# Kernel optimization log

Measured on AMD Instinct MI355X. Metric: run time of the kernel, lower is better.

Reference implementation:

```python
import jax, jax.numpy as jnp
import numpy as np

EPS = 1e-6
NEG_SLOPE = 0.2

B, C_IN, N, K = 4, 64, 40960, 16
C_OUT = 64


def setup_inputs() -> dict:
    key = jax.random.key(0)
    k1, k2, k3 = jax.random.split(key, 3)
    feature = jax.random.normal(k1, (B, C_IN, N, 1), dtype=jnp.float32)
    neigh_idx = jax.random.randint(k2, (B, N, K), 0, N, dtype=jnp.int64)
    # 1x1 conv kernel [C_out, C_in] (kaiming-like scale), no bias since bn=True
    W = jax.random.normal(k3, (C_OUT, C_IN), dtype=jnp.float32) * np.float32(np.sqrt(2.0 / C_IN))
    gamma = jnp.ones((C_OUT,), dtype=jnp.float32)
    beta = jnp.zeros((C_OUT,), dtype=jnp.float32)
    return {"feature": feature, "W": W, "gamma": gamma, "beta": beta, "neigh_idx": neigh_idx}


def _gather_neighbour(pc, neigh_idx):
    # pc: [B, C, N]; neigh_idx: [B, N, K] -> [B, C, N, K]
    return jax.vmap(lambda p, idx: p[:, idx])(pc, neigh_idx)


def reference(feature, W, gamma, beta, neigh_idx):
    pc = feature[..., 0]                       # [B, C, N]
    f_neigh = _gather_neighbour(pc, neigh_idx) # [B, C, N, K]
    x = jnp.concatenate([feature, f_neigh], axis=-1)  # [B, C, N, K+1]
    # 1x1 conv (no bias)
    y = jnp.einsum('oc,bcnk->bonk', W, x)      # [B, C_out, N, K+1]
    # BatchNorm2d (training mode: batch stats over B,N,K+1), eps=1e-6
    mean = jnp.mean(y, axis=(0, 2, 3), keepdims=True)
    var = jnp.mean(jnp.square(y - mean), axis=(0, 2, 3), keepdims=True)
    yn = (y - mean) * jax.lax.rsqrt(var + EPS)
    yn = yn * gamma[None, :, None, None] + beta[None, :, None, None]
    # LeakyReLU(0.2)
    act = jnp.where(yn >= 0, yn, NEG_SLOPE * yn)
    # sum over neighbor axis, keepdim
    return jnp.sum(act, axis=-1, keepdims=True)  # [B, C_out, N, 1]
```

## Files before the change

### kernel.cpp

```cpp
#include <hip/hip_runtime.h>
#include <hip/hip_fp16.h>

typedef _Float16 h2 __attribute__((ext_vector_type(2)));

#define BB 4
#define CIN 64
#define COUT 64
#define NN 40960
#define KK 16
#define GBLK (BB * NN / 256)
#define FPAD 264
#define WPAD 68
#define HP 32
#define HR 2
#define HBINS (NN / HR)
#define HWORDS (HBINS / 4)

__global__ __launch_bounds__(256) void k_hist(const int* __restrict__ idx,
                                              unsigned int* __restrict__ hist,
                                              float* __restrict__ sums) {
    __shared__ unsigned int bins[HWORDS];
    const int tid = threadIdx.x;
    const int p = blockIdx.x >> 3;
    const int b = (blockIdx.x & 7) >> 1;
    const int r = blockIdx.x & 1;
    const int lo = r * HBINS;

    if (blockIdx.x == 0 && tid < 128) sums[tid] = 0.f;

#pragma unroll
    for (int i = 0; i < HWORDS / 256; ++i) bins[i * 256 + tid] = 0u;
    __syncthreads();

    const int SHARE = NN * KK / HP;
    const int4* src = (const int4*)(idx + (size_t)b * NN * KK + (size_t)p * SHARE);
#pragma unroll 4
    for (int i = 0; i < SHARE / 4 / 256; ++i) {
        int4 v = src[i * 256 + tid];
        unsigned a0 = (unsigned)(v.x - lo), a1 = (unsigned)(v.y - lo);
        unsigned a2 = (unsigned)(v.z - lo), a3 = (unsigned)(v.w - lo);
        if (a0 < HBINS) atomicAdd(&bins[a0 >> 2], 1u << ((a0 & 3) * 8));
        if (a1 < HBINS) atomicAdd(&bins[a1 >> 2], 1u << ((a1 & 3) * 8));
        if (a2 < HBINS) atomicAdd(&bins[a2 >> 2], 1u << ((a2 & 3) * 8));
        if (a3 < HBINS) atomicAdd(&bins[a3 >> 2], 1u << ((a3 & 3) * 8));
    }
    __syncthreads();
    unsigned int* dst = hist + (size_t)((b * HP + p) * HR + r) * HWORDS;
#pragma unroll
    for (int i = 0; i < HWORDS / 256; ++i) dst[i * 256 + tid] = bins[i * 256 + tid];
}

__global__ __launch_bounds__(256) void k_gemm(const float* __restrict__ feat,
                                              const float* __restrict__ W,
                                              const unsigned int* __restrict__ hist,
                                              __half* __restrict__ g,
                                              float* __restrict__ sums) {
    __shared__ float Wt_s[64 * WPAD];
    __shared__ float feat_s[16 * FPAD];
    __shared__ float w_s[256];

    const int tid   = threadIdx.x;
    const int b     = (blockIdx.x & 7) >> 1;
    const int chunk = (blockIdx.x & 1) * 80 + (blockIdx.x >> 3);
    const int n0    = chunk * 256;

    {
        const int n  = n0 + tid;
        const int r  = n / HBINS;
        const int ml = n - r * HBINS;
        const int w  = ml >> 2;
        const int sh = (ml & 3) * 8;
        unsigned s = 1u;
#pragma unroll
        for (int p = 0; p < HP; ++p)
            s += (hist[(size_t)((b * HP + p) * HR + r) * HWORDS + w] >> sh) & 0xffu;
        w_s[tid] = (float)s;
    }

#pragma unroll
    for (int it = 0; it < 16; ++it) {
        int c = tid & 63;
        int o = it * 4 + (tid >> 6);
        Wt_s[c * WPAD + o] = W[o * 64 + c];
    }

    const int to = tid & 7;
    const int tn = tid >> 3;

    float acc[8][8];
#pragma unroll
    for (int i = 0; i < 8; ++i)
#pragma unroll
        for (int j = 0; j < 8; ++j) acc[i][j] = 0.f;

    const float* fb = feat + (size_t)b * CIN * NN + n0;

    for (int cc0 = 0; cc0 < 64; cc0 += 16) {
        __syncthreads();
        {
            int row = tid >> 4;
            int col = (tid & 15) * 4;
            const float* src = fb + (size_t)(cc0 + row) * NN + col;
#pragma unroll
            for (int q = 0; q < 4; ++q) {
                float4 v = *(const float4*)(src + q * 64);
                *(float4*)&feat_s[row * FPAD + col + q * 64] = v;
            }
        }
        __syncthreads();

#pragma unroll
        for (int cc = 0; cc < 16; ++cc) {
            int c = cc0 + cc;
            float4 w0 = *(const float4*)&Wt_s[c * WPAD + to * 8];
            float4 w1 = *(const float4*)&Wt_s[c * WPAD + to * 8 + 4];
            float4 f0 = *(const float4*)&feat_s[cc * FPAD + tn * 8];
            float4 f1 = *(const float4*)&feat_s[cc * FPAD + tn * 8 + 4];
            float wv[8] = {w0.x, w0.y, w0.z, w0.w, w1.x, w1.y, w1.z, w1.w};
            float fv[8] = {f0.x, f0.y, f0.z, f0.w, f1.x, f1.y, f1.z, f1.w};
#pragma unroll
            for (int i = 0; i < 8; ++i)
#pragma unroll
                for (int j = 0; j < 8; ++j)
                    acc[i][j] = fmaf(wv[i], fv[j], acc[i][j]);
        }
    }

    __half* gb = g + ((size_t)b * NN + n0) * 64;
#pragma unroll
    for (int j = 0; j < 8; ++j) {
        int n = tn * 8 + j;
        union { uint4 u; h2 h[4]; } P;
#pragma unroll
        for (int h = 0; h < 4; ++h) {
            h2 t;
            t.x = (_Float16)acc[2 * h][j];
            t.y = (_Float16)acc[2 * h + 1][j];
            P.h[h] = t;
        }
        *(uint4*)&gb[(size_t)n * 64 + to * 8] = P.u;
    }

    float wgt[8];
#pragma unroll
    for (int j = 0; j < 8; ++j) wgt[j] = w_s[tn * 8 + j];
    float s1[8], s2[8];
#pragma unroll
    for (int i = 0; i < 8; ++i) { s1[i] = 0.f; s2[i] = 0.f; }
#pragma unroll
    for (int j = 0; j < 8; ++j)
#pragma unroll
        for (int i = 0; i < 8; ++i) {
            float wv = wgt[j] * acc[i][j];
            s1[i] += wv;
            s2[i] += wv * acc[i][j];
        }

    __syncthreads();
    float* red = feat_s;
#pragma unroll
    for (int i = 0; i < 8; ++i) {
        int o = to * 8 + i;
        red[o * 33 + tn]        = s1[i];
        red[2112 + o * 33 + tn] = s2[i];
    }
    __syncthreads();
    if (tid < 128) {
        int arr = tid >> 6, o = tid & 63;
        const float* base = red + arr * 2112 + o * 33;
        float s = 0.f;
#pragma unroll
        for (int t = 0; t < 32; ++t) s += base[t];
        atomicAdd(&sums[arr * 64 + o], s);
    }
}

__global__ __launch_bounds__(256) void k_final(const __half* __restrict__ g,
                                               const int* __restrict__ idx,
                                               const float* __restrict__ sums,
                                               const float* __restrict__ gamma,
                                               const float* __restrict__ beta,
                                               float* __restrict__ out) {
    const int tid  = threadIdx.x;
    const int lane = tid & 63;
    const int wave = tid >> 6;
    const int b     = (blockIdx.x & 7) >> 1;
    const int chunk = ((blockIdx.x >> 3) << 1) | (blockIdx.x & 1);
    const int n0    = chunk * 64;

    __shared__ int   idx_s[64 * 17];
    __shared__ float tile[64 * 65];
    __shared__ float prm[128];

    {
        const int4* src = (const int4*)(idx + ((size_t)b * NN + n0) * KK);
        int4 v = src[tid];
        int row = tid >> 2, col = (tid & 3) * 4;
        idx_s[row * 17 + col + 0] = v.x;
        idx_s[row * 17 + col + 1] = v.y;
        idx_s[row * 17 + col + 2] = v.z;
        idx_s[row * 17 + col + 3] = v.w;
    }

    if (tid < 64) {
        const double TOT = (double)BB * NN * (KK + 1);
        double mean = (double)sums[tid] / TOT;
        double var  = (double)sums[64 + tid] / TOT - mean * mean;
        double inv  = 1.0 / sqrt(var + 1e-6);
        float scale = (float)inv * gamma[tid];
        float shift = beta[tid] - (float)mean * scale;
        prm[tid]      = scale;
        prm[64 + tid] = shift;
    }
    __syncthreads();

    const int r  = lane >> 3;
    const int q8 = (lane & 7) * 8;
    h2 sc2[4], sh2[4];
#pragma unroll
    for (int h = 0; h < 4; ++h) {
        h2 a, s;
        a.x = (_Float16)prm[q8 + 2 * h];      a.y = (_Float16)prm[q8 + 2 * h + 1];
        s.x = (_Float16)prm[64 + q8 + 2 * h]; s.y = (_Float16)prm[64 + q8 + 2 * h + 1];
        sc2[h] = a; sh2[h] = s;
    }

    const __half* gb = g + (size_t)b * NN * 64;

#pragma unroll
    for (int rr = 0; rr < 2; ++rr) {
        const int nl = wave * 16 + rr * 8 + r;
        h2 acc[4];
#pragma unroll
        for (int h = 0; h < 4; ++h) acc[h] = (h2)(_Float16)0;

#pragma unroll
        for (int k = -1; k < KK; ++k) {
            int m = (k < 0) ? (n0 + nl) : idx_s[nl * 17 + k];
            union { uint4 u; h2 h[4]; } U;
            U.u = *(const uint4*)(gb + (size_t)m * 64 + q8);
#pragma unroll
            for (int h = 0; h < 4; ++h) {
                h2 t = U.h[h] * sc2[h] + sh2[h];
                acc[h] += __builtin_elementwise_max(t, t * (_Float16)0.2f);
            }
        }
        float* tr = &tile[nl * 65 + q8];
#pragma unroll
        for (int h = 0; h < 4; ++h) {
            tr[2 * h]     = (float)acc[h].x;
            tr[2 * h + 1] = (float)acc[h].y;
        }
    }
    __syncthreads();
    const int j   = tid & 63;
    const int sub = tid >> 6;
#pragma unroll
    for (int ob = 0; ob < 16; ++ob) {
        int o = ob * 4 + sub;
        out[(size_t)(b * 64 + o) * NN + n0 + j] = tile[j * 65 + o];
    }
}

extern "C" void kernel_launch(void* const* d_in, const int* in_sizes, int n_in,
                              void* d_out, int out_size, void* d_ws, size_t ws_size,
                              hipStream_t stream) {
    const float* feat  = (const float*)d_in[0];
    const float* W     = (const float*)d_in[1];
    const float* gamma = (const float*)d_in[2];
    const float* beta  = (const float*)d_in[3];
    const int*   idx   = (const int*)d_in[4];
    float* out = (float*)d_out;

    char* ws = (char*)d_ws;
    __half* g = (__half*)ws;
    size_t off = (size_t)BB * NN * 64 * sizeof(__half);
    unsigned int* hist = (unsigned int*)(ws + off);
    off += (size_t)BB * HP * HR * HWORDS * sizeof(unsigned int);
    float* sums = (float*)(ws + off);

    k_hist<<<BB * HP * HR, 256, 0, stream>>>(idx, hist, sums);
    k_gemm<<<GBLK, 256, 0, stream>>>(feat, W, hist, g, sums);
    k_final<<<(BB * NN) / 64, 256, 0, stream>>>(g, idx, sums, gamma, beta, out);
}
```

Before: 155.3 us.

## Split neighbour gathers into two index-range passes and use nontemporal idx/out access

The final kernel now gathers neighbour rows in two passes, each touching only neighbours whose index falls in one half of the point range. This is meant to shrink the live working set of the fp16 feature table so it stays resident in cache. Index loads and output stores become nontemporal so they do not evict the gathered table. The cost is a branch per neighbour, accumulators held for both rows at once, and divergent lanes inside each pass.

After: 186.3 us. 1.2x slower.

```diff
diff --git a/kernel.cpp b/kernel.cpp
--- a/kernel.cpp
+++ b/kernel.cpp
@@ -2,6 +2,7 @@
 #include <hip/hip_fp16.h>
 
 typedef _Float16 h2 __attribute__((ext_vector_type(2)));
+typedef unsigned int u32x4 __attribute__((ext_vector_type(4)));
 
 #define BB 4
 #define CIN 64
@@ -193,13 +194,13 @@
     __shared__ float prm[128];
 
     {
-        const int4* src = (const int4*)(idx + ((size_t)b * NN + n0) * KK);
-        int4 v = src[tid];
+        const u32x4* src = (const u32x4*)(idx + ((size_t)b * NN + n0) * KK);
+        u32x4 v = __builtin_nontemporal_load(src + tid);
         int row = tid >> 2, col = (tid & 3) * 4;
-        idx_s[row * 17 + col + 0] = v.x;
-        idx_s[row * 17 + col + 1] = v.y;
-        idx_s[row * 17 + col + 2] = v.z;
-        idx_s[row * 17 + col + 3] = v.w;
+        idx_s[row * 17 + col + 0] = (int)v.x;
+        idx_s[row * 17 + col + 1] = (int)v.y;
+        idx_s[row * 17 + col + 2] = (int)v.z;
+        idx_s[row * 17 + col + 3] = (int)v.w;
     }
 
     if (tid < 64) {
@@ -227,29 +228,43 @@
 
     const __half* gb = g + (size_t)b * NN * 64;
 
+    h2 acc[2][4];
+#pragma unroll
+    for (int rr = 0; rr < 2; ++rr)
+#pragma unroll
+        for (int h = 0; h < 4; ++h) acc[rr][h] = (h2)(_Float16)0;
+
+#pragma unroll
+    for (int pass = 0; pass < 2; ++pass) {
+        const int mlo = pass * (NN / 2);
+#pragma unroll
+        for (int rr = 0; rr < 2; ++rr) {
+            const int nl = wave * 16 + rr * 8 + r;
+#pragma unroll
+            for (int k = -1; k < KK; ++k) {
+                int m = (k < 0) ? (n0 + nl) : idx_s[nl * 17 + k];
+                if ((unsigned)(m - mlo) < (unsigned)(NN / 2)) {
+                    union { uint4 u; h2 h[4]; } U;
+                    U.u = *(const uint4*)(gb + (size_t)m * 64 + q8);
+#pragma unroll
+                    for (int h = 0; h < 4; ++h) {
+                        h2 t = U.h[h] * sc2[h] + sh2[h];
+                        acc[rr][h] += __builtin_elementwise_max(t, t * (_Float16)0.2f);
+                    }
+                }
+            }
+        }
+        __builtin_amdgcn_sched_barrier(0);
+    }
+
 #pragma unroll
     for (int rr = 0; rr < 2; ++rr) {
         const int nl = wave * 16 + rr * 8 + r;
-        h2 acc[4];
-#pragma unroll
-        for (int h = 0; h < 4; ++h) acc[h] = (h2)(_Float16)0;
-
-#pragma unroll
-        for (int k = -1; k < KK; ++k) {
-            int m = (k < 0) ? (n0 + nl) : idx_s[nl * 17 + k];
-            union { uint4 u; h2 h[4]; } U;
-            U.u = *(const uint4*)(gb + (size_t)m * 64 + q8);
-#pragma unroll
-            for (int h = 0; h < 4; ++h) {
-                h2 t = U.h[h] * sc2[h] + sh2[h];
-                acc[h] += __builtin_elementwise_max(t, t * (_Float16)0.2f);
-            }
-        }
         float* tr = &tile[nl * 65 + q8];
 #pragma unroll
         for (int h = 0; h < 4; ++h) {
-            tr[2 * h]     = (float)acc[h].x;
-            tr[2 * h + 1] = (float)acc[h].y;
+            tr[2 * h]     = (float)acc[rr][h].x;
+            tr[2 * h + 1] = (float)acc[rr][h].y;
         }
     }
     __syncthreads();
@@ -258,7 +273,8 @@
 #pragma unroll
     for (int ob = 0; ob < 16; ++ob) {
         int o = ob * 4 + sub;
-        out[(size_t)(b * 64 + o) * NN + n0 + j] = tile[j * 65 + o];
+        __builtin_nontemporal_store(tile[j * 65 + o],
+                                    &out[(size_t)(b * 64 + o) * NN + n0 + j]);
     }
 }
 
```

## Use fp16 MFMA for pointwise conv GEMM and add nontemporal idx/out accesses

Applied to the files above, without the earlier changes.

Replaces the fp32 register-tiled FMA GEMM in k_gemm with fp16 MFMA 16x16x32 instructions. W is loaded directly into fragments, and feature values are converted to half straight from global memory without an LDS staging loop. Results go through a padded LDS tile so the g stores stay coalesced, and the BN-stat reduction is reworked to match the MFMA output layout. k_final also switches the neighbour-index loads and output stores to nontemporal hints. Rounding the inputs and weights to fp16 before the matmul lowers precision of y and the batch statistics, and the feature loads become strided scalar reads.

Measured after the change: 158.4 us. 1.02x slower.

```diff
diff --git a/kernel.cpp b/kernel.cpp
--- a/kernel.cpp
+++ b/kernel.cpp
@@ -2,6 +2,9 @@
 #include <hip/hip_fp16.h>
 
 typedef _Float16 h2 __attribute__((ext_vector_type(2)));
+typedef _Float16 f16x8 __attribute__((ext_vector_type(8)));
+typedef float f32x4 __attribute__((ext_vector_type(4)));
+typedef unsigned int u32x4 __attribute__((ext_vector_type(4)));
 
 #define BB 4
 #define CIN 64
@@ -9,12 +12,11 @@
 #define NN 40960
 #define KK 16
 #define GBLK (BB * NN / 256)
-#define FPAD 264
-#define WPAD 68
 #define HP 32
 #define HR 2
 #define HBINS (NN / HR)
 #define HWORDS (HBINS / 4)
+#define GTP 72
 
 __global__ __launch_bounds__(256) void k_hist(const int* __restrict__ idx,
                                               unsigned int* __restrict__ hist,
@@ -55,9 +57,9 @@
                                               const unsigned int* __restrict__ hist,
                                               __half* __restrict__ g,
                                               float* __restrict__ sums) {
-    __shared__ float Wt_s[64 * WPAD];
-    __shared__ float feat_s[16 * FPAD];
-    __shared__ float w_s[256];
+    __shared__ __half gt[4][64][GTP];
+    __shared__ float  red[2][64][17];
+    __shared__ float  w_s[256];
 
     const int tid   = threadIdx.x;
     const int b     = (blockIdx.x & 7) >> 1;
@@ -77,101 +79,102 @@
         w_s[tid] = (float)s;
     }
 
-#pragma unroll
-    for (int it = 0; it < 16; ++it) {
-        int c = tid & 63;
-        int o = it * 4 + (tid >> 6);
-        Wt_s[c * WPAD + o] = W[o * 64 + c];
-    }
-
-    const int to = tid & 7;
-    const int tn = tid >> 3;
-
-    float acc[8][8];
-#pragma unroll
-    for (int i = 0; i < 8; ++i)
-#pragma unroll
-        for (int j = 0; j < 8; ++j) acc[i][j] = 0.f;
-
-    const float* fb = feat + (size_t)b * CIN * NN + n0;
-
-    for (int cc0 = 0; cc0 < 64; cc0 += 16) {
-        __syncthreads();
-        {
-            int row = tid >> 4;
-            int col = (tid & 15) * 4;
-            const float* src = fb + (size_t)(cc0 + row) * NN + col;
-#pragma unroll
-            for (int q = 0; q < 4; ++q) {
-                float4 v = *(const float4*)(src + q * 64);
-                *(float4*)&feat_s[row * FPAD + col + q * 64] = v;
+    const int wv = tid >> 6;
+    const int l  = tid & 63;
+    const int lr = l & 15;
+    const int lg = l >> 4;
+
+    f16x8 bf[2][4];
+#pragma unroll
+    for (int ot = 0; ot < 4; ++ot)
+#pragma unroll
+        for (int kc = 0; kc < 2; ++kc) {
+            const float* wp = W + (size_t)(ot * 16 + lr) * 64 + kc * 32 + lg * 8;
+            float4 w0 = *(const float4*)(wp);
+            float4 w1 = *(const float4*)(wp + 4);
+            f16x8 t;
+            t[0] = (_Float16)w0.x; t[1] = (_Float16)w0.y;
+            t[2] = (_Float16)w0.z; t[3] = (_Float16)w0.w;
+            t[4] = (_Float16)w1.x; t[5] = (_Float16)w1.y;
+            t[6] = (_Float16)w1.z; t[7] = (_Float16)w1.w;
+            bf[kc][ot] = t;
+        }
+
+    f32x4 acc[4][4];
+#pragma unroll
+    for (int i = 0; i < 4; ++i)
+#pragma unroll
+        for (int j = 0; j < 4; ++j) acc[i][j] = (f32x4)0.f;
+
+    const float* fb = feat + (size_t)b * CIN * NN;
+    const int nbase = n0 + wv * 64;
+
+#pragma unroll
+    for (int nt = 0; nt < 4; ++nt) {
+        const int n = nbase + nt * 16 + lr;
+#pragma unroll
+        for (int kc = 0; kc < 2; ++kc) {
+            const float* ap = fb + (size_t)(kc * 32 + lg * 8) * NN + n;
+            f16x8 a;
+#pragma unroll
+            for (int j = 0; j < 8; ++j) a[j] = (_Float16)ap[(size_t)j * NN];
+#pragma unroll
+            for (int ot = 0; ot < 4; ++ot)
+                acc[nt][ot] = __builtin_amdgcn_mfma_f32_16x16x32_f16(
+                    a, bf[kc][ot], acc[nt][ot], 0, 0, 0);
+        }
+    }
+
+    float wr[4][4];
+#pragma unroll
+    for (int nt = 0; nt < 4; ++nt)
+#pragma unroll
+        for (int r = 0; r < 4; ++r)
+            wr[nt][r] = w_s[wv * 64 + nt * 16 + lg * 4 + r];
+
+    float s1[4] = {0.f, 0.f, 0.f, 0.f}, s2[4] = {0.f, 0.f, 0.f, 0.f};
+#pragma unroll
+    for (int nt = 0; nt < 4; ++nt)
+#pragma unroll
+        for (int ot = 0; ot < 4; ++ot)
+#pragma unroll
+            for (int r = 0; r < 4; ++r) {
+                float y = acc[nt][ot][r];
+                float t = wr[nt][r] * y;
+                s1[ot] += t;
+                s2[ot] += t * y;
             }
-        }
-        __syncthreads();
-
-#pragma unroll
-        for (int cc = 0; cc < 16; ++cc) {
-            int c = cc0 + cc;
-            float4 w0 = *(const float4*)&Wt_s[c * WPAD + to * 8];
-            float4 w1 = *(const float4*)&Wt_s[c * WPAD + to * 8 + 4];
-            float4 f0 = *(const float4*)&feat_s[cc * FPAD + tn * 8];
-            float4 f1 = *(const float4*)&feat_s[cc * FPAD + tn * 8 + 4];
-            float wv[8] = {w0.x, w0.y, w0.z, w0.w, w1.x, w1.y, w1.z, w1.w};
-            float fv[8] = {f0.x, f0.y, f0.z, f0.w, f1.x, f1.y, f1.z, f1.w};
-#pragma unroll
-            for (int i = 0; i < 8; ++i)
-#pragma unroll
-                for (int j = 0; j < 8; ++j)
-                    acc[i][j] = fmaf(wv[i], fv[j], acc[i][j]);
-        }
-    }
+
+#pragma unroll
+    for (int nt = 0; nt < 4; ++nt)
+#pragma unroll
+        for (int ot = 0; ot < 4; ++ot)
+#pragma unroll
+            for (int r = 0; r < 4; ++r)
+                gt[wv][nt * 16 + lg * 4 + r][ot * 16 + lr] = (__half)acc[nt][ot][r];
+
+#pragma unroll
+    for (int ot = 0; ot < 4; ++ot) {
+        red[0][ot * 16 + lr][wv * 4 + lg] = s1[ot];
+        red[1][ot * 16 + lr][wv * 4 + lg] = s2[ot];
+    }
+    __syncthreads();
 
     __half* gb = g + ((size_t)b * NN + n0) * 64;
 #pragma unroll
-    for (int j = 0; j < 8; ++j) {
-        int n = tn * 8 + j;
-        union { uint4 u; h2 h[4]; } P;
-#pragma unroll
-        for (int h = 0; h < 4; ++h) {
-            h2 t;
-            t.x = (_Float16)acc[2 * h][j];
-            t.y = (_Float16)acc[2 * h + 1][j];
-            P.h[h] = t;
-        }
-        *(uint4*)&gb[(size_t)n * 64 + to * 8] = P.u;
-    }
-
-    float wgt[8];
-#pragma unroll
-    for (int j = 0; j < 8; ++j) wgt[j] = w_s[tn * 8 + j];
-    float s1[8], s2[8];
-#pragma unroll
-    for (int i = 0; i < 8; ++i) { s1[i] = 0.f; s2[i] = 0.f; }
-#pragma unroll
-    for (int j = 0; j < 8; ++j)
-#pragma unroll
-        for (int i = 0; i < 8; ++i) {
-            float wv = wgt[j] * acc[i][j];
-            s1[i] += wv;
-            s2[i] += wv * acc[i][j];
-        }
-
-    __syncthreads();
-    float* red = feat_s;
-#pragma unroll
     for (int i = 0; i < 8; ++i) {
-        int o = to * 8 + i;
-        red[o * 33 + tn]        = s1[i];
-        red[2112 + o * 33 + tn] = s2[i];
-    }
-    __syncthreads();
+        int nl = i * 32 + (tid >> 3);
+        int o8 = (tid & 7) * 8;
+        uint4 v = *(const uint4*)&gt[nl >> 6][nl & 63][o8];
+        *(uint4*)&gb[(size_t)nl * 64 + o8] = v;
+    }
+
     if (tid < 128) {
-        int arr = tid >> 6, o = tid & 63;
-        const float* base = red + arr * 2112 + o * 33;
-        float s = 0.f;
-#pragma unroll
-        for (int t = 0; t < 32; ++t) s += base[t];
-        atomicAdd(&sums[arr * 64 + o], s);
+        int s = tid >> 6, o = tid & 63;
+        float acc_s = 0.f;
+#pragma unroll
+        for (int t = 0; t < 16; ++t) acc_s += red[s][o][t];
+        atomicAdd(&sums[s * 64 + o], acc_s);
     }
 }
 
@@ -193,13 +196,13 @@
     __shared__ float prm[128];
 
     {
-        const int4* src = (const int4*)(idx + ((size_t)b * NN + n0) * KK);
-        int4 v = src[tid];
+        const u32x4* src = (const u32x4*)(idx + ((size_t)b * NN + n0) * KK);
+        u32x4 v = __builtin_nontemporal_load(src + tid);
         int row = tid >> 2, col = (tid & 3) * 4;
-        idx_s[row * 17 + col + 0] = v.x;
-        idx_s[row * 17 + col + 1] = v.y;
-        idx_s[row * 17 + col + 2] = v.z;
-        idx_s[row * 17 + col + 3] = v.w;
+        idx_s[row * 17 + col + 0] = (int)v.x;
+        idx_s[row * 17 + col + 1] = (int)v.y;
+        idx_s[row * 17 + col + 2] = (int)v.z;
+        idx_s[row * 17 + col + 3] = (int)v.w;
     }
 
     if (tid < 64) {
@@ -258,7 +261,8 @@
 #pragma unroll
     for (int ob = 0; ob < 16; ++ob) {
         int o = ob * 4 + sub;
-        out[(size_t)(b * 64 + o) * NN + n0 + j] = tile[j * 65 + o];
+        __builtin_nontemporal_store(tile[j * 65 + o],
+                                    &out[(size_t)(b * 64 + o) * NN + n0 + j]);
     }
 }
 
```
